# Performance work log

Hardware: AMD Instinct MI355X
Metric: run time of the kernel (lower is better)

Reference implementation:

```python
import jax, jax.numpy as jnp
import numpy as np

VOCAB, EMB, HID, FC1, NCLS = 32000, 2048, 2048, 256, 3
T, B = 256, 128


def setup_inputs() -> dict:
    key = jax.random.key(0)
    ks = jax.random.split(key, 10)
    s_e = 1.0  # torch Embedding default init N(0,1)
    s_h = 1.0 / np.sqrt(HID)
    s_f1 = 1.0 / np.sqrt(HID)
    s_f2 = 1.0 / np.sqrt(FC1)
    return {
        "x": jax.random.randint(ks[0], (T, B), 0, VOCAB, dtype=jnp.int64)
        if jax.config.jax_enable_x64 else jax.random.randint(ks[0], (T, B), 0, VOCAB, dtype=jnp.int32),
        "emb": jax.random.normal(ks[1], (VOCAB, EMB), dtype=jnp.float32) * s_e,
        "W_ih": jax.random.uniform(ks[2], (HID, EMB), jnp.float32, -s_h, s_h),
        "W_hh": jax.random.uniform(ks[3], (HID, HID), jnp.float32, -s_h, s_h),
        "b_ih": jax.random.uniform(ks[4], (HID,), jnp.float32, -s_h, s_h),
        "b_hh": jax.random.uniform(ks[5], (HID,), jnp.float32, -s_h, s_h),
        "fc1_w": jax.random.uniform(ks[6], (FC1, HID), jnp.float32, -s_f1, s_f1),
        "fc1_b": jax.random.uniform(ks[7], (FC1,), jnp.float32, -s_f1, s_f1),
        "fc2_w": jax.random.uniform(ks[8], (NCLS, FC1), jnp.float32, -s_f2, s_f2),
        "fc2_b": jax.random.uniform(ks[9], (NCLS,), jnp.float32, -s_f2, s_f2),
    }


def reference(x, emb, W_ih, W_hh, b_ih, b_hh, fc1_w, fc1_b, fc2_w, fc2_b):
    # Embedding: [T, B] -> [T, B, E]
    xe = emb[x]
    # Precompute input projections for all steps in one big GEMM: [T, B, H]
    xproj = jnp.einsum("tbe,he->tbh", xe, W_ih) + b_ih + b_hh
    h0 = jnp.zeros((x.shape[1], W_hh.shape[0]), dtype=xe.dtype)

    def step(h, xp_t):
        h = jnp.tanh(xp_t + h @ W_hh.T)
        return h, None

    h_last, _ = jax.lax.scan(step, h0, xproj)
    # MLP head: hidden -> 256 -> relu -> 3
    z = jax.nn.relu(h_last @ fc1_w.T + fc1_b)
    return z @ fc2_w.T + fc2_b
```

## Files before the change

kernel.cpp:

```cpp
#include <hip/hip_runtime.h>

typedef _Float16 half8 __attribute__((ext_vector_type(8)));
typedef _Float16 half4v __attribute__((ext_vector_type(4)));
typedef float float4v __attribute__((ext_vector_type(4)));

#define HID 2048
#define EMBD 2048
#define BATCH 128
#define TSTEPS 256
#define STEP ((size_t)BATCH * HID)

__global__ __launch_bounds__(256) void cast_f16_kernel(const float* __restrict__ src,
                                                       _Float16* __restrict__ dst, int n) {
    int i = (blockIdx.x * 256 + threadIdx.x) * 4;
    int stride = gridDim.x * 256 * 4;
    for (; i < n; i += stride) {
        float4v v = *(const float4v*)(src + i);
        half4v h;
        h[0] = (_Float16)v[0]; h[1] = (_Float16)v[1];
        h[2] = (_Float16)v[2]; h[3] = (_Float16)v[3];
        *(half4v*)(dst + i) = h;
    }
}

__global__ __launch_bounds__(256) void bias_kernel(const float* __restrict__ a,
                                                   const float* __restrict__ b,
                                                   float* __restrict__ dst) {
    int i = blockIdx.x * 256 + threadIdx.x;
    if (i < HID) dst[i] = a[i] + b[i];
}

__global__ __launch_bounds__(256) void phaseA_kernel(const int* __restrict__ x,
                                                     const float* __restrict__ emb,
                                                     const _Float16* __restrict__ w16,
                                                     const float* __restrict__ bias,
                                                     _Float16* __restrict__ xproj) {
    __shared__ __align__(16) _Float16 As[128 * 64];
    __shared__ __align__(16) _Float16 Bs[128 * 64];

    const int tid = threadIdx.x;
    const int bx  = blockIdx.x;
    const int nt = bx & 15, mt = bx >> 4;
    const long m0 = (long)mt * 128;
    const long n0 = (long)nt * 128;
    const int lane = tid & 63, w = tid >> 6;
    const int ln15 = lane & 15, kg = lane >> 4;
    const int wr = (w >> 1) * 64, wc = (w & 1) * 64;

    int xr[4];
#pragma unroll
    for (int it = 0; it < 4; ++it) xr[it] = x[m0 + ((it * 256 + tid) >> 3)];

    float4v acc[4][4];
#pragma unroll
    for (int m = 0; m < 4; ++m)
#pragma unroll
        for (int n = 0; n < 4; ++n) acc[m][n] = (float4v){0.f, 0.f, 0.f, 0.f};

    for (int kt = 0; kt < 32; ++kt) {
        __syncthreads();
#pragma unroll
        for (int it = 0; it < 4; ++it) {
            int c = it * 256 + tid;
            const float* src = emb + (long)xr[it] * EMBD + kt * 64 + (c & 7) * 8;
            float4v v0 = *(const float4v*)src;
            float4v v1 = *(const float4v*)(src + 4);
            half8 hv;
#pragma unroll
            for (int q = 0; q < 4; ++q) { hv[q] = (_Float16)v0[q]; hv[4 + q] = (_Float16)v1[q]; }
            *(half8*)(&As[c * 8]) = hv;
        }
#pragma unroll
        for (int it = 0; it < 4; ++it) {
            int c = it * 256 + tid;
            const _Float16* src = w16 + (n0 + (c >> 3)) * (long)EMBD + kt * 64 + (c & 7) * 8;
            *(half8*)(&Bs[c * 8]) = *(const half8*)src;
        }
        __syncthreads();
#pragma unroll
        for (int kk = 0; kk < 2; ++kk) {
            half8 a[4], b[4];
#pragma unroll
            for (int m = 0; m < 4; ++m)
                a[m] = *(half8*)(&As[(wr + m * 16 + ln15) * 64 + kk * 32 + kg * 8]);
#pragma unroll
            for (int n = 0; n < 4; ++n)
                b[n] = *(half8*)(&Bs[(wc + n * 16 + ln15) * 64 + kk * 32 + kg * 8]);
#pragma unroll
            for (int m = 0; m < 4; ++m)
#pragma unroll
                for (int n = 0; n < 4; ++n)
                    acc[m][n] = __builtin_amdgcn_mfma_f32_16x16x32_f16(b[n], a[m], acc[m][n], 0, 0, 0);
        }
    }
#pragma unroll
    for (int m = 0; m < 4; ++m) {
        long mg = m0 + wr + m * 16 + ln15;
#pragma unroll
        for (int n = 0; n < 4; ++n) {
            int nb = (int)n0 + wc + n * 16 + kg * 4;
            float4v bv = *(const float4v*)(bias + nb);
            union { half4v h; unsigned long long u; } pk;
#pragma unroll
            for (int r = 0; r < 4; ++r) pk.h[r] = (_Float16)(acc[m][n][r] + bv[r]);
            *(unsigned long long*)(xproj + mg * HID + nb) = pk.u;
        }
    }
}

__global__ __launch_bounds__(256, 1) void scan_kernel(_Float16* __restrict__ xproj,
                                                      const _Float16* __restrict__ whh,
                                                      const _Float16* __restrict__ h0,
                                                      float* __restrict__ hlast,
                                                      unsigned* __restrict__ flags) {
    __shared__ __align__(16) _Float16 Wl[32 * 2048];
    __shared__ __align__(16) float part[4][16 * 40];

    const int tid = threadIdx.x;
    const int bx = blockIdx.x;
    const int gid = bx & 3;
    const int sub = bx >> 2;
    const int m0 = gid * 32;
    const int n0 = sub * 32;
    const int lane = tid & 63, w = tid >> 6;
    const int ln15 = lane & 15, kg = lane >> 4;
    const int pr = w >> 1;
    const int kh = w & 1;

    for (int it = 0; it < 32; ++it) {
        int c = it * 256 + tid;
        int col = c >> 8;
        int ch = c & 255;
        half8 v = *(const half8*)(whh + (long)(n0 + col) * HID + ch * 8);
        *(half8*)((char*)Wl + col * 4096 + ((ch * 16) ^ ((col & 7) << 4))) = v;
    }
    __syncthreads();

    unsigned* gfl = flags + gid * 64;
    const int rp = tid >> 7;
    const int ridx = tid & 127;
    const int rrow = ridx >> 3;
    const int rc4 = (ridx & 7) * 4;
    const int grow = m0 + rp * 16 + rrow;
    const int gcol = n0 + rc4;

    const int wb0 = ln15 * 4096;
    const int wb1 = (16 + ln15) * 4096;
    const int swz = (ln15 & 7) << 4;
    const int kb = kh * 2048;
    const int arow = m0 + pr * 16 + ln15;

    for (int t = 0; t < TSTEPS; ++t) {
        const _Float16* hcur = (t == 0) ? h0 : xproj + (size_t)(t - 1) * STEP;
        _Float16* hnext = xproj + (size_t)t * STEP;

        unsigned long long xbits = __hip_atomic_load(
            (const unsigned long long*)(xproj + (size_t)t * STEP + (size_t)grow * HID + gcol),
            __ATOMIC_RELAXED, __HIP_MEMORY_SCOPE_AGENT);

        const _Float16* hrow = hcur + (size_t)arow * HID + kh * 1024;
        float4v acc0 = (float4v){0.f, 0.f, 0.f, 0.f};
        float4v acc1 = (float4v){0.f, 0.f, 0.f, 0.f};
#pragma unroll
        for (int ki = 0; ki < 32; ++ki) {
            half8 a = *(const half8*)(hrow + ki * 32 + kg * 8);
            int k2 = kb + ki * 64 + kg * 16;
            half8 b0 = *(half8*)((char*)Wl + wb0 + (k2 ^ swz));
            half8 b1 = *(half8*)((char*)Wl + wb1 + (k2 ^ swz));
            acc0 = __builtin_amdgcn_mfma_f32_16x16x32_f16(a, b0, acc0, 0, 0, 0);
            acc1 = __builtin_amdgcn_mfma_f32_16x16x32_f16(a, b1, acc1, 0, 0, 0);
        }

#pragma unroll
        for (int r = 0; r < 4; ++r) {
            part[w][(kg * 4 + r) * 40 + ln15] = acc0[r];
            part[w][(kg * 4 + r) * 40 + 16 + ln15] = acc1[r];
        }
        __syncthreads();

        float4v s = *(const float4v*)(&part[2 * rp][rrow * 40 + rc4]) +
                    *(const float4v*)(&part[2 * rp + 1][rrow * 40 + rc4]);
        union { unsigned long long u; half4v h; } xb; xb.u = xbits;
        float o0 = tanhf(s[0] + (float)xb.h[0]);
        float o1 = tanhf(s[1] + (float)xb.h[1]);
        float o2 = tanhf(s[2] + (float)xb.h[2]);
        float o3 = tanhf(s[3] + (float)xb.h[3]);
        union { half4v h; unsigned long long u; } pk;
        pk.h[0] = (_Float16)o0; pk.h[1] = (_Float16)o1;
        pk.h[2] = (_Float16)o2; pk.h[3] = (_Float16)o3;
        __hip_atomic_store((unsigned long long*)(hnext + (size_t)grow * HID + gcol), pk.u,
                           __ATOMIC_RELAXED, __HIP_MEMORY_SCOPE_AGENT);
        if (t == TSTEPS - 1) {
            float4v f = {o0, o1, o2, o3};
            *(float4v*)(hlast + (size_t)grow * HID + gcol) = f;
            break;
        }

        __syncthreads();
        if (tid == 0)
            __hip_atomic_store(&gfl[sub], (unsigned)(t + 1),
                               __ATOMIC_RELAXED, __HIP_MEMORY_SCOPE_AGENT);
        if (tid < 32) {
            const unsigned long long* pp = (const unsigned long long*)gfl + tid;
            for (;;) {
                unsigned long long v = __hip_atomic_load(pp, __ATOMIC_RELAXED,
                                                         __HIP_MEMORY_SCOPE_AGENT);
                bool ok = ((unsigned)v > (unsigned)t) && ((unsigned)(v >> 32) > (unsigned)t);
                if (__all(ok)) break;
                __builtin_amdgcn_s_sleep(2);
            }
        }
        __syncthreads();
    }
}

__global__ __launch_bounds__(256) void fc1_kernel(const float* __restrict__ hlast,
                                                  const float* __restrict__ w,
                                                  const float* __restrict__ b,
                                                  float* __restrict__ z) {
    int bb = blockIdx.x;
    int j = threadIdx.x;
    const float* hr = hlast + (long)bb * HID;
    const float* wr = w + (long)j * HID;
    float acc = 0.f;
    for (int k = 0; k < HID; k += 4) {
        float4v hv = *(const float4v*)(hr + k);
        float4v wv = *(const float4v*)(wr + k);
        acc += hv[0] * wv[0] + hv[1] * wv[1] + hv[2] * wv[2] + hv[3] * wv[3];
    }
    acc += b[j];
    z[bb * 256 + j] = fmaxf(acc, 0.f);
}

__global__ __launch_bounds__(256) void fc2_kernel(const float* __restrict__ z,
                                                  const float* __restrict__ w,
                                                  const float* __restrict__ b,
                                                  float* __restrict__ out) {
    __shared__ float red[4];
    int bb = blockIdx.x;
    int tid = threadIdx.x;
    float zv = z[bb * 256 + tid];
    for (int c = 0; c < 3; ++c) {
        float s = zv * w[c * 256 + tid];
        for (int off = 32; off > 0; off >>= 1) s += __shfl_down(s, off, 64);
        if ((tid & 63) == 0) red[tid >> 6] = s;
        __syncthreads();
        if (tid == 0) out[bb * 3 + c] = red[0] + red[1] + red[2] + red[3] + b[c];
        __syncthreads();
    }
}

extern "C" void kernel_launch(void* const* d_in, const int* in_sizes, int n_in,
                              void* d_out, int out_size, void* d_ws, size_t ws_size,
                              hipStream_t stream) {
    const int*   x    = (const int*)d_in[0];
    const float* emb  = (const float*)d_in[1];
    const float* Wih  = (const float*)d_in[2];
    const float* Whh  = (const float*)d_in[3];
    const float* bih  = (const float*)d_in[4];
    const float* bhh  = (const float*)d_in[5];
    const float* fc1w = (const float*)d_in[6];
    const float* fc1b = (const float*)d_in[7];
    const float* fc2w = (const float*)d_in[8];
    const float* fc2b = (const float*)d_in[9];
    float* out = (float*)d_out;

    char* ws = (char*)d_ws;
    size_t off = 0;
    _Float16* xproj = (_Float16*)(ws + off); off += (size_t)TSTEPS * BATCH * HID * 2;
    _Float16* wih16 = (_Float16*)(ws + off); off += (size_t)HID * EMBD * 2;
    _Float16* whh16 = (_Float16*)(ws + off); off += (size_t)HID * HID * 2;
    float*    bias  = (float*)(ws + off);    off += (size_t)HID * 4;
    _Float16* h0    = (_Float16*)(ws + off); off += (size_t)BATCH * HID * 2;
    float*    hlast = (float*)(ws + off);    off += (size_t)BATCH * HID * 4;
    float*    z     = (float*)(ws + off);    off += (size_t)BATCH * 256 * 4;
    unsigned* flags = (unsigned*)(ws + off); off += 4 * 64 * 4;

    hipMemsetAsync(flags, 0, 4 * 64 * 4, stream);
    hipMemsetAsync(h0, 0, (size_t)BATCH * HID * 2, stream);

    cast_f16_kernel<<<4096, 256, 0, stream>>>(Wih, wih16, HID * EMBD);
    cast_f16_kernel<<<4096, 256, 0, stream>>>(Whh, whh16, HID * HID);
    bias_kernel<<<8, 256, 0, stream>>>(bih, bhh, bias);

    phaseA_kernel<<<4096, 256, 0, stream>>>(x, emb, wih16, bias, xproj);

    void* args[] = {(void*)&xproj, (void*)&whh16, (void*)&h0, (void*)&hlast, (void*)&flags};
    hipLaunchCooperativeKernel((const void*)scan_kernel, dim3(256), dim3(256), args, 0, stream);

    fc1_kernel<<<BATCH, 256, 0, stream>>>(hlast, fc1w, fc1b, z);
    fc2_kernel<<<BATCH, 256, 0, stream>>>(z, fc2w, fc2b, out);
}
```

Measured before the change: 2.735 ms.

## Replace per-step grid barrier with fine-grained per-chunk flags and poller wave

The scan kernel gets a dedicated fifth wave that polls per-wave global progress flags and mirrors per-K-chunk minima into LDS. Compute waves then wait only on the 128-column chunk of h they need before issuing MFMAs. This replaces the all-block barrier per timestep and removes the split-K LDS reduction, since each wave now owns a full-K 16x16 tile. Step 0 skips the matmul entirely, so the zero h0 buffer and its memset are gone. The trade is more flag traffic, spin-waiting on LDS and relaxed-ordering subtleties, in exchange for letting dependent work start before the whole step finishes.

```diff
diff --git a/kernel.cpp b/kernel.cpp
--- a/kernel.cpp
+++ b/kernel.cpp
@@ -108,13 +108,12 @@
     }
 }
 
-__global__ __launch_bounds__(256, 1) void scan_kernel(_Float16* __restrict__ xproj,
+__global__ __launch_bounds__(320, 1) void scan_kernel(_Float16* __restrict__ xproj,
                                                       const _Float16* __restrict__ whh,
-                                                      const _Float16* __restrict__ h0,
                                                       float* __restrict__ hlast,
                                                       unsigned* __restrict__ flags) {
     __shared__ __align__(16) _Float16 Wl[32 * 2048];
-    __shared__ __align__(16) float part[4][16 * 40];
+    __shared__ unsigned ldsflag[32];
 
     const int tid = threadIdx.x;
     const int bx = blockIdx.x;
@@ -124,93 +123,88 @@
     const int n0 = sub * 32;
     const int lane = tid & 63, w = tid >> 6;
     const int ln15 = lane & 15, kg = lane >> 4;
-    const int pr = w >> 1;
-    const int kh = w & 1;
-
-    for (int it = 0; it < 32; ++it) {
-        int c = it * 256 + tid;
-        int col = c >> 8;
-        int ch = c & 255;
+
+    for (int c = tid; c < 8192; c += 320) {
+        int col = c >> 8, ch = c & 255;
         half8 v = *(const half8*)(whh + (long)(n0 + col) * HID + ch * 8);
         *(half8*)((char*)Wl + col * 4096 + ((ch * 16) ^ ((col & 7) << 4))) = v;
     }
+    if (tid < 32) ldsflag[tid] = 0;
     __syncthreads();
 
-    unsigned* gfl = flags + gid * 64;
-    const int rp = tid >> 7;
-    const int ridx = tid & 127;
-    const int rrow = ridx >> 3;
-    const int rc4 = (ridx & 7) * 4;
-    const int grow = m0 + rp * 16 + rrow;
-    const int gcol = n0 + rc4;
-
-    const int wb0 = ln15 * 4096;
-    const int wb1 = (16 + ln15) * 4096;
+    unsigned* gfl = flags + gid * 256;
+
+    if (w == 4) {
+        if (lane < 32) {
+            const unsigned long long* fp = (const unsigned long long*)gfl + (size_t)lane * 4;
+            unsigned m = 0;
+            while (m < TSTEPS - 1) {
+                unsigned long long v0 = __hip_atomic_load(fp + 0, __ATOMIC_RELAXED, __HIP_MEMORY_SCOPE_AGENT);
+                unsigned long long v1 = __hip_atomic_load(fp + 1, __ATOMIC_RELAXED, __HIP_MEMORY_SCOPE_AGENT);
+                unsigned long long v2 = __hip_atomic_load(fp + 2, __ATOMIC_RELAXED, __HIP_MEMORY_SCOPE_AGENT);
+                unsigned long long v3 = __hip_atomic_load(fp + 3, __ATOMIC_RELAXED, __HIP_MEMORY_SCOPE_AGENT);
+                unsigned a0 = (unsigned)v0, a1 = (unsigned)(v0 >> 32);
+                unsigned a2 = (unsigned)v1, a3 = (unsigned)(v1 >> 32);
+                unsigned a4 = (unsigned)v2, a5 = (unsigned)(v2 >> 32);
+                unsigned a6 = (unsigned)v3, a7 = (unsigned)(v3 >> 32);
+                unsigned mn = min(min(min(a0, a1), min(a2, a3)), min(min(a4, a5), min(a6, a7)));
+                m = mn;
+                __hip_atomic_store(&ldsflag[lane], m, __ATOMIC_RELAXED, __HIP_MEMORY_SCOPE_WORKGROUP);
+            }
+        }
+        return;
+    }
+
+    const int qr = w >> 1, qc = w & 1;
+    const size_t arow = (size_t)(m0 + qr * 16 + ln15);
+    const int wbyte = (qc * 16 + ln15) * 4096;
     const int swz = (ln15 & 7) << 4;
-    const int kb = kh * 2048;
-    const int arow = m0 + pr * 16 + ln15;
-
-    for (int t = 0; t < TSTEPS; ++t) {
-        const _Float16* hcur = (t == 0) ? h0 : xproj + (size_t)(t - 1) * STEP;
-        _Float16* hnext = xproj + (size_t)t * STEP;
-
+    const int ocol = n0 + qc * 16 + kg * 4;
+    const int fidx = qr * 128 + (sub >> 2) * 8 + (sub & 3) * 2 + qc;
+    unsigned* myflags = &ldsflag[qr * 16];
+
+    for (int s = 0; s < TSTEPS; ++s) {
         unsigned long long xbits = __hip_atomic_load(
-            (const unsigned long long*)(xproj + (size_t)t * STEP + (size_t)grow * HID + gcol),
+            (const unsigned long long*)(xproj + (size_t)s * STEP + arow * HID + ocol),
             __ATOMIC_RELAXED, __HIP_MEMORY_SCOPE_AGENT);
 
-        const _Float16* hrow = hcur + (size_t)arow * HID + kh * 1024;
-        float4v acc0 = (float4v){0.f, 0.f, 0.f, 0.f};
-        float4v acc1 = (float4v){0.f, 0.f, 0.f, 0.f};
-#pragma unroll
-        for (int ki = 0; ki < 32; ++ki) {
-            half8 a = *(const half8*)(hrow + ki * 32 + kg * 8);
-            int k2 = kb + ki * 64 + kg * 16;
-            half8 b0 = *(half8*)((char*)Wl + wb0 + (k2 ^ swz));
-            half8 b1 = *(half8*)((char*)Wl + wb1 + (k2 ^ swz));
-            acc0 = __builtin_amdgcn_mfma_f32_16x16x32_f16(a, b0, acc0, 0, 0, 0);
-            acc1 = __builtin_amdgcn_mfma_f32_16x16x32_f16(a, b1, acc1, 0, 0, 0);
-        }
-
-#pragma unroll
-        for (int r = 0; r < 4; ++r) {
-            part[w][(kg * 4 + r) * 40 + ln15] = acc0[r];
-            part[w][(kg * 4 + r) * 40 + 16 + ln15] = acc1[r];
-        }
-        __syncthreads();
-
-        float4v s = *(const float4v*)(&part[2 * rp][rrow * 40 + rc4]) +
-                    *(const float4v*)(&part[2 * rp + 1][rrow * 40 + rc4]);
+        float4v acc = (float4v){0.f, 0.f, 0.f, 0.f};
+        if (s > 0) {
+            const _Float16* hrow = xproj + (size_t)(s - 1) * STEP + arow * HID;
+            for (int j = 0; j < 16; ++j) {
+                while (__hip_atomic_load(&myflags[j], __ATOMIC_ACQUIRE,
+                                         __HIP_MEMORY_SCOPE_WORKGROUP) < (unsigned)s) {}
+                __builtin_amdgcn_sched_barrier(0);
+#pragma unroll
+                for (int ki = 0; ki < 4; ++ki) {
+                    int k = j * 128 + ki * 32;
+                    half8 a = *(const half8*)(hrow + k + kg * 8);
+                    half8 b = *(half8*)((char*)Wl + wbyte + ((k * 2 + kg * 16) ^ swz));
+                    acc = __builtin_amdgcn_mfma_f32_16x16x32_f16(b, a, acc, 0, 0, 0);
+                }
+            }
+        }
+
         union { unsigned long long u; half4v h; } xb; xb.u = xbits;
-        float o0 = tanhf(s[0] + (float)xb.h[0]);
-        float o1 = tanhf(s[1] + (float)xb.h[1]);
-        float o2 = tanhf(s[2] + (float)xb.h[2]);
-        float o3 = tanhf(s[3] + (float)xb.h[3]);
-        union { half4v h; unsigned long long u; } pk;
-        pk.h[0] = (_Float16)o0; pk.h[1] = (_Float16)o1;
-        pk.h[2] = (_Float16)o2; pk.h[3] = (_Float16)o3;
-        __hip_atomic_store((unsigned long long*)(hnext + (size_t)grow * HID + gcol), pk.u,
-                           __ATOMIC_RELAXED, __HIP_MEMORY_SCOPE_AGENT);
-        if (t == TSTEPS - 1) {
+        float o0 = tanhf(acc[0] + (float)xb.h[0]);
+        float o1 = tanhf(acc[1] + (float)xb.h[1]);
+        float o2 = tanhf(acc[2] + (float)xb.h[2]);
+        float o3 = tanhf(acc[3] + (float)xb.h[3]);
+
+        if (s < TSTEPS - 1) {
+            union { half4v h; unsigned long long u; } pk;
+            pk.h[0] = (_Float16)o0; pk.h[1] = (_Float16)o1;
+            pk.h[2] = (_Float16)o2; pk.h[3] = (_Float16)o3;
+            __hip_atomic_store((unsigned long long*)(xproj + (size_t)s * STEP + arow * HID + ocol),
+                               pk.u, __ATOMIC_RELAXED, __HIP_MEMORY_SCOPE_AGENT);
+            asm volatile("s_waitcnt vmcnt(0)" ::: "memory");
+            if (lane == 0)
+                __hip_atomic_store(&gfl[fidx], (unsigned)(s + 1),
+                                   __ATOMIC_RELAXED, __HIP_MEMORY_SCOPE_AGENT);
+        } else {
             float4v f = {o0, o1, o2, o3};
-            *(float4v*)(hlast + (size_t)grow * HID + gcol) = f;
-            break;
-        }
-
-        __syncthreads();
-        if (tid == 0)
-            __hip_atomic_store(&gfl[sub], (unsigned)(t + 1),
-                               __ATOMIC_RELAXED, __HIP_MEMORY_SCOPE_AGENT);
-        if (tid < 32) {
-            const unsigned long long* pp = (const unsigned long long*)gfl + tid;
-            for (;;) {
-                unsigned long long v = __hip_atomic_load(pp, __ATOMIC_RELAXED,
-                                                         __HIP_MEMORY_SCOPE_AGENT);
-                bool ok = ((unsigned)v > (unsigned)t) && ((unsigned)(v >> 32) > (unsigned)t);
-                if (__all(ok)) break;
-                __builtin_amdgcn_s_sleep(2);
-            }
-        }
-        __syncthreads();
+            *(float4v*)(hlast + arow * HID + ocol) = f;
+        }
     }
 }
 
@@ -271,13 +265,11 @@
     _Float16* wih16 = (_Float16*)(ws + off); off += (size_t)HID * EMBD * 2;
     _Float16* whh16 = (_Float16*)(ws + off); off += (size_t)HID * HID * 2;
     float*    bias  = (float*)(ws + off);    off += (size_t)HID * 4;
-    _Float16* h0    = (_Float16*)(ws + off); off += (size_t)BATCH * HID * 2;
     float*    hlast = (float*)(ws + off);    off += (size_t)BATCH * HID * 4;
     float*    z     = (float*)(ws + off);    off += (size_t)BATCH * 256 * 4;
-    unsigned* flags = (unsigned*)(ws + off); off += 4 * 64 * 4;
-
-    hipMemsetAsync(flags, 0, 4 * 64 * 4, stream);
-    hipMemsetAsync(h0, 0, (size_t)BATCH * HID * 2, stream);
+    unsigned* flags = (unsigned*)(ws + off); off += 4 * 256 * 4;
+
+    hipMemsetAsync(flags, 0, 4 * 256 * 4, stream);
 
     cast_f16_kernel<<<4096, 256, 0, stream>>>(Wih, wih16, HID * EMBD);
     cast_f16_kernel<<<4096, 256, 0, stream>>>(Whh, whh16, HID * HID);
@@ -285,8 +277,8 @@
 
     phaseA_kernel<<<4096, 256, 0, stream>>>(x, emb, wih16, bias, xproj);
 
-    void* args[] = {(void*)&xproj, (void*)&whh16, (void*)&h0, (void*)&hlast, (void*)&flags};
-    hipLaunchCooperativeKernel((const void*)scan_kernel, dim3(256), dim3(256), args, 0, stream);
+    void* args[] = {(void*)&xproj, (void*)&whh16, (void*)&hlast, (void*)&flags};
+    hipLaunchCooperativeKernel((const void*)scan_kernel, dim3(256), dim3(320), args, 0, stream);
 
     fc1_kernel<<<BATCH, 256, 0, stream>>>(hlast, fc1w, fc1b, z);
     fc2_kernel<<<BATCH, 256, 0, stream>>>(z, fc2w, fc2b, out);
```

New measurement: 4.692 ms. 71.5% more time.
